# Optimization experiments

Hardware: AMD Instinct MI355X
Metric: run time of the kernel (lower is better)

## Reference

```python
import jax, jax.numpy as jnp
import numpy as np

R = 40000      # aug_num_rels
E = 500000     # number of relation-graph triplets
DIN = 64       # rel_emb_dim
DH = 64        # hid_dim_rel
H = 8          # num_head
DHID = DH // H # 8
NBIN = 10
L = 2          # num_layer_rel


def _leaky(x):
    return jax.nn.leaky_relu(x, negative_slope=0.2)


def _rel_layer(emb_rel, head, tail, binidx, pw, pb, abin, avec, aw, ab):
    # emb_rel: [R, DH]; head/tail/binidx: [E]
    concat = jnp.concatenate([emb_rel[head], emb_rel[tail]], axis=-1)  # [E, 2*DH]
    z = _leaky(concat @ pw + pb).reshape(-1, H, DHID)                   # [E, H, DHID]
    # attention logits: per-head dot with attn_vec + leaky(bin bias)
    raw = (z * avec[None]).sum(-1) + _leaky(abin[binidx, :, 0])         # [E, H]
    # segmented softmax over edges grouped by head index
    m = jax.ops.segment_max(raw, head, num_segments=R)                  # [R, H]
    e = jnp.exp(raw - m[head])                                          # [E, H]
    s = jax.ops.segment_sum(e, head, num_segments=R)                    # [R, H]
    beta = e / (s[head] + 1e-16)                                        # [E, H]
    msg = (emb_rel[tail] @ aw + ab).reshape(-1, H, DHID) * beta[..., None]
    out = jax.ops.segment_sum(msg, head, num_segments=R)                # [R, H, DHID]
    return out.reshape(R, DH)


def setup_inputs() -> dict:
    key = jax.random.key(0)
    ks = jax.random.split(key, 12)
    ht = jax.random.randint(ks[0], (E, 2), 0, R)
    b = jax.random.randint(ks[1], (E, 1), 0, NBIN)
    relation_triplets = jnp.concatenate([ht, b], axis=-1).astype(jnp.int64)
    sc = 0.05
    return {
        "relation_triplets": relation_triplets,
        "rel_emb_w": jax.random.normal(ks[2], (R, DIN), jnp.float32) * sc,
        "proj1_w": jax.random.normal(ks[3], (DIN, DH), jnp.float32) * sc,
        "proj1_b": jnp.zeros((DH,), jnp.float32),
        "attn_proj_w": jax.random.normal(ks[4], (L, 2 * DH, DH), jnp.float32) * sc,
        "attn_proj_b": jnp.zeros((L, DH), jnp.float32),
        "attn_bin": jax.random.normal(ks[5], (L, NBIN, H, 1), jnp.float32) * sc,
        "attn_vec": jax.random.normal(ks[6], (L, H, DHID), jnp.float32) * sc,
        "aggr_w": jax.random.normal(ks[7], (L, DH, DH), jnp.float32) * sc,
        "aggr_b": jnp.zeros((L, DH), jnp.float32),
        "res_w": jax.random.normal(ks[8], (L, DH, DH), jnp.float32) * sc,
        "res_b": jnp.zeros((L, DH), jnp.float32),
    }


def reference(relation_triplets, rel_emb_w, proj1_w, proj1_b, attn_proj_w,
              attn_proj_b, attn_bin, attn_vec, aggr_w, aggr_b, res_w, res_b):
    head = relation_triplets[:, 0]
    tail = relation_triplets[:, 1]
    binidx = relation_triplets[:, 2]
    emb_rel = jax.nn.relu(rel_emb_w @ proj1_w + proj1_b)  # [R, DH]
    for l in range(L):
        h = _rel_layer(emb_rel, head, tail, binidx,
                       attn_proj_w[l], attn_proj_b[l], attn_bin[l],
                       attn_vec[l], aggr_w[l], aggr_b[l])
        h = jax.nn.relu(h)
        emb_rel = h + jax.nn.relu(emb_rel @ res_w[l] + res_b[l])
    return emb_rel
```

## Files before the change

kernel.cpp:

```cpp
#include <hip/hip_runtime.h>
#include <hip/hip_bf16.h>

typedef __hip_bfloat16 bf16;

#define R_NUM 40000
#define E_NUM 500000
#define HIST_BLOCKS 1954
#define XF_BLOCKS 1250

#define PK_P1 0
#define PK_P1B 4096
#define PK_XF 4160
#define PK_AB 36928
#define PK_APB 37056
#define PK_RB 37184
#define PK_ABIN 37312
#define PK_AVEC 37472
#define PK_END 37600
#define PACK_BLOCKS 147

#define N_CNTS 0
#define N_ROWP 160000
#define N_RANK 320256
#define N_STB 2320384
#define N_FLAG 4320640
#define N_WBUF 4320896
#define N_XMP0 4471296
#define N_HR0 14711296
#define N_XMP1 35191296
#define N_HR1 45431296
#define NEED2 65911296ull

#define W_P1W 0
#define W_P1B 4096
#define W_APW 4160
#define W_APB 20544
#define W_ABIN 20672
#define W_AVEC 20832
#define W_AW 20960
#define W_AB 29152
#define W_RW 29280
#define W_RB 37472
#define W_END 37600
#define WCONV_BLOCKS 147

#define O_FLAG 0
#define O_WBUF 256
#define O_ROWP 150784
#define O_CNTS 310784
#define O_STB 635136
#define O_BIG 2635392

static __device__ __forceinline__ float b2f(bf16 x) { return __bfloat162float(x); }
static __device__ __forceinline__ float ldv(const float* p, size_t i) { return p[i]; }
static __device__ __forceinline__ float ldv(const bf16* p, size_t i) { return __bfloat162float(p[i]); }
static __device__ __forceinline__ void stv(float* p, size_t i, float v) { p[i] = v; }
static __device__ __forceinline__ void stv(bf16* p, size_t i, float v) { p[i] = __float2bfloat16(v); }

static __device__ __forceinline__ unsigned int f2bb(float x) {
  union { float f; unsigned int u; } v;
  v.f = x;
  unsigned int r = v.u + 0x7FFFu + ((v.u >> 16) & 1u);
  return r >> 16;
}
static __device__ __forceinline__ unsigned int packxm(float xt, float mt) {
  return f2bb(xt) | (f2bb(mt) << 16);
}

static __device__ __forceinline__ void load_edge(const unsigned int* __restrict__ w, int e,
                                                 int i64, int& h, int& t, int& b) {
  if (i64) {
    h = (int)w[6 * e + 0];
    t = (int)w[6 * e + 2];
    b = (int)w[6 * e + 4];
  } else {
    h = (int)w[3 * e + 0];
    t = (int)w[3 * e + 1];
    b = (int)w[3 * e + 2];
  }
}


__global__ void k_detect_init(const unsigned int* __restrict__ trip_w,
                              const unsigned short* __restrict__ emb_w, int* __restrict__ flag,
                              int* __restrict__ counts, int* __restrict__ stb) {
  int tid = threadIdx.x;
  if (blockIdx.x == 0) {
    if (tid < 64) {
      int lane = tid;
      unsigned int acc = 0;
      for (int i = lane; i < 1024; i += 64) acc |= trip_w[2 * i + 1];
      int votes = 0;
      for (int i = lane; i < 2048; i += 64) {
        unsigned short u = emb_w[2 * i];
        int ex = (u >> 7) & 0xFF;
        if (ex >= 90 && ex <= 130) votes++;
      }
      for (int off = 1; off < 64; off <<= 1) {
        acc |= __shfl_xor(acc, off);
        votes += __shfl_xor(votes, off);
      }
      if (lane == 0) {
        flag[0] = (acc == 0) ? 1 : 0;
        flag[1] = (votes < 1024) ? 1 : 0;
      }
    }
    return;
  }
  int g = (blockIdx.x - 1) * 256 + tid;
  for (int i = g; i < R_NUM; i += 159 * 256) counts[i] = 0;
  if (blockIdx.x == 1 && tid < 64) stb[E_NUM + tid] = 0;
}


__global__ void k_pack(const int* __restrict__ flag, const void* p1w, const void* p1b,
                       const void* apw, const void* apb, const void* abin, const void* avec,
                       const void* aw, const void* ab, const void* rw, const void* rb,
                       float* __restrict__ wbuf) {
  int i = blockIdx.x * 256 + threadIdx.x;
  if (i >= PK_END) return;
  const void* src;
  int off;
  if (i < PK_P1B) {
    int g = i >> 8, r = i & 255, j = r >> 2, di = r & 3;
    src = p1w;
    off = (g * 4 + di) * 64 + j;
  } else if (i < PK_XF) {
    src = p1b;
    off = i - PK_P1B;
  } else if (i < PK_AB) {
    int t = i - PK_XF;
    int l = t >> 14;
    t &= 16383;
    int g = t >> 10;
    t &= 1023;
    int m = t >> 8;
    int r = t & 255, j = r >> 2, di = r & 3;
    int ii = g * 4 + di;
    if (m == 0) { src = apw; off = l * 8192 + 4096 + ii * 64 + j; }
    else if (m == 1) { src = aw; off = l * 4096 + ii * 64 + j; }
    else if (m == 2) { src = apw; off = l * 8192 + ii * 64 + j; }
    else { src = rw; off = l * 4096 + ii * 64 + j; }
  } else if (i < PK_APB) { src = ab; off = i - PK_AB; }
  else if (i < PK_RB) { src = apb; off = i - PK_APB; }
  else if (i < PK_ABIN) { src = rb; off = i - PK_RB; }
  else if (i < PK_AVEC) { src = abin; off = i - PK_ABIN; }
  else { src = avec; off = i - PK_AVEC; }
  wbuf[i] = flag[1] ? ((const float*)src)[off] : b2f(((const bf16*)src)[off]);
}


static __device__ __forceinline__ void xf4p(const float (*sW)[64], int j, int l,
                                            const float* __restrict__ wbuf, int r0,
                                            unsigned int* __restrict__ XMp,
                                            float2* __restrict__ HR) {
  const float* W = wbuf + PK_XF + l * 16384;
  float axt[8] = {};
  float amt[8] = {};
  float axh[8] = {};
  float ars[8] = {};
  for (int g = 0; g < 16; g++) {
    const float* Wg = W + g * 1024 + j * 4;
    float4 w0 = *(const float4*)&Wg[0];
    float4 w1 = *(const float4*)&Wg[256];
    float4 w2 = *(const float4*)&Wg[512];
    float4 w3 = *(const float4*)&Wg[768];
    float4 ev[8];
#pragma unroll
    for (int n = 0; n < 8; n++) ev[n] = *(const float4*)&sW[n][g * 4];
#pragma unroll
    for (int di = 0; di < 4; di++) {
      float wt = ((const float*)&w0)[di];
      float wm = ((const float*)&w1)[di];
      float wh = ((const float*)&w2)[di];
      float wr = ((const float*)&w3)[di];
#pragma unroll
      for (int n = 0; n < 8; n++) {
        float e = ((const float*)&ev[n])[di];
        axt[n] = fmaf(e, wt, axt[n]);
        amt[n] = fmaf(e, wm, amt[n]);
        axh[n] = fmaf(e, wh, axh[n]);
        ars[n] = fmaf(e, wr, ars[n]);
      }
    }
  }
  float abj = wbuf[PK_AB + l * 64 + j];
  float pbj = wbuf[PK_APB + l * 64 + j];
  float rbj = wbuf[PK_RB + l * 64 + j];
#pragma unroll
  for (int n = 0; n < 8; n++) {
    XMp[(size_t)(r0 + n) * 64 + j] = packxm(axt[n], amt[n] + abj);
    HR[(size_t)(r0 + n) * 64 + j] = make_float2(axh[n] + pbj, fmaxf(ars[n] + rbj, 0.f));
  }
}


template <typename T>
static __device__ __forceinline__ void kA_xform(const T* __restrict__ A,
                                                const float* __restrict__ wbuf, int r0,
                                                unsigned int* __restrict__ XMp0,
                                                float2* __restrict__ HR0, float (*sW)[64]) {
  int j = threadIdx.x & 63;
  for (int k = j; k < 512; k += 64) {
    int rr = k >> 6, cc = k & 63;
    sW[rr][cc] = ldv(A, (size_t)(r0 + rr) * 64 + cc);
  }
  float a[8] = {0.f, 0.f, 0.f, 0.f, 0.f, 0.f, 0.f, 0.f};
  const float* P1 = wbuf + PK_P1;
  for (int g = 0; g < 16; g++) {
    float4 wv4 = *(const float4*)&P1[g * 256 + j * 4];
    float4 ev[8];
#pragma unroll
    for (int n = 0; n < 8; n++) ev[n] = *(const float4*)&sW[n][g * 4];
#pragma unroll
    for (int di = 0; di < 4; di++) {
      float wv = ((const float*)&wv4)[di];
#pragma unroll
      for (int n = 0; n < 8; n++) a[n] = fmaf(((const float*)&ev[n])[di], wv, a[n]);
    }
  }
  float bj = wbuf[PK_P1B + j];
#pragma unroll
  for (int n = 0; n < 8; n++) {
    a[n] = fmaxf(a[n] + bj, 0.f);
    sW[n][j] = a[n];
  }
  xf4p((const float(*)[64])sW, j, 0, wbuf, r0, XMp0, HR0);
}

__global__ void __launch_bounds__(256, 4) kA(const unsigned int* __restrict__ trip_w,
                                             const int* __restrict__ flag,
                                             const void* __restrict__ A,
                                             const float* __restrict__ wbuf,
                                             int* __restrict__ counts, int* __restrict__ rank,
                                             unsigned int* __restrict__ XMp0,
                                             float2* __restrict__ HR0) {
  if (blockIdx.x >= XF_BLOCKS) {
    int e = (blockIdx.x - XF_BLOCKS) * 256 + threadIdx.x;
    if (e < E_NUM) {
      int h = flag[0] ? (int)trip_w[6 * e] : (int)trip_w[3 * e];
      rank[e] = atomicAdd(&counts[h], 1);
    }
    return;
  }
  __shared__ float sA[32][64];
  int w = threadIdx.x >> 6;
  int r0 = blockIdx.x * 32 + w * 8;
  float(*sW)[64] = (float(*)[64]) & sA[w * 8][0];
  if (flag[1])
    kA_xform<float>((const float*)A, wbuf, r0, XMp0, HR0, sW);
  else
    kA_xform<bf16>((const bf16*)A, wbuf, r0, XMp0, HR0, sW);
}


__global__ void __launch_bounds__(1024) k_scan1(const int* __restrict__ counts,
                                                int* __restrict__ row_ptr) {
  __shared__ int sp[1024];
  int tid = threadIdx.x;
  int base = tid * 40;
  int local[40];
  int s = 0;
  if (base < R_NUM) {
#pragma unroll
    for (int k = 0; k < 40; k++) {
      int v = counts[base + k];
      local[k] = s;
      s += v;
    }
  }
  sp[tid] = s;
  __syncthreads();
  for (int off = 1; off < 1024; off <<= 1) {
    int t = (tid >= off) ? sp[tid - off] : 0;
    __syncthreads();
    sp[tid] += t;
    __syncthreads();
  }
  int pre = (tid == 0) ? 0 : sp[tid - 1];
  if (base < R_NUM) {
#pragma unroll
    for (int k = 0; k < 40; k++) row_ptr[base + k] = pre + local[k];
  }
  if (tid == 1023) row_ptr[R_NUM] = sp[1023];
}

__global__ void k_scatter2(const unsigned int* __restrict__ trip_w, const int* __restrict__ flag,
                           const int* __restrict__ row_ptr, const int* __restrict__ rank,
                           int* __restrict__ stb) {
  int e = blockIdx.x * 256 + threadIdx.x;
  if (e >= E_NUM) return;
  int h, t, b;
  load_edge(trip_w, e, flag[0], h, t, b);
  int pos = row_ptr[h] + rank[e];
  stb[pos] = (t & 0xFFFF) | (b << 16);
}


static __device__ __forceinline__ void edge_body(int l, const int* __restrict__ row_ptr,
                                                 const int* __restrict__ stb,
                                                 const unsigned int* __restrict__ XMp,
                                                 const float2* __restrict__ HR,
                                                 const float* __restrict__ wbuf,
                                                 float* __restrict__ out, float* sab) {
  int tid = threadIdx.x;
  int lane = tid & 63;
  int w = tid >> 6;
  int hh = lane >> 3;
  if (tid < 80) {
    float a = wbuf[PK_ABIN + l * 80 + tid];
    sab[tid] = (a > 0.f) ? a : 0.2f * a;
  }
  __syncthreads();
  float av = wbuf[PK_AVEC + l * 64 + lane];

  int r = blockIdx.x * 4 + w;
  float2 hr = HR[(size_t)r * 64 + lane];
  int beg = row_ptr[r];
  int end = row_ptr[r + 1];
  beg = __builtin_amdgcn_readfirstlane(beg);
  end = __builtin_amdgcn_readfirstlane(end);

  float xh = hr.x;
  float num = 0.f, den = 0.f;
  int t0 = (beg < end) ? (stb[beg] & 0xFFFF) : 0;
  for (int jj = beg; jj < end; jj += 16) {
    int pk[16];
    unsigned int xp[16];
#pragma unroll
    for (int k = 0; k < 16; k++) pk[k] = stb[jj + k];
#pragma unroll
    for (int k = 0; k < 16; k++) {
      int t = (jj + k < end) ? (pk[k] & 0xFFFF) : t0;
      xp[k] = XMp[(size_t)t * 64 + lane];
    }
#pragma unroll
    for (int k = 0; k < 16; k++) {
      float xt = __uint_as_float(xp[k] << 16);
      float mt = __uint_as_float(xp[k] & 0xFFFF0000u);
      float z = xh + xt;
      z = (z > 0.f) ? z : 0.2f * z;
      float v = z * av;
      v += __shfl_xor(v, 1);
      v += __shfl_xor(v, 2);
      v += __shfl_xor(v, 4);
      float e = __expf(v + sab[(pk[k] >> 16) * 8 + hh]);
      e = (jj + k < end) ? e : 0.f;
      den += e;
      num = fmaf(mt, e, num);
    }
  }
  out[(size_t)r * 64 + lane] = fmaxf(num / (den + 1e-16f), 0.f) + hr.y;
}

__global__ void __launch_bounds__(256, 8) kE0(const int* __restrict__ row_ptr,
                                              const int* __restrict__ stb,
                                              const unsigned int* __restrict__ XMp0,
                                              const float2* __restrict__ HR0,
                                              const float* __restrict__ wbuf,
                                              float* __restrict__ emb) {
  __shared__ float sab[80];
  edge_body(0, row_ptr, stb, XMp0, HR0, wbuf, emb, sab);
}

__global__ void __launch_bounds__(256, 8) kC(const int* __restrict__ row_ptr,
                                             const int* __restrict__ stb,
                                             const unsigned int* __restrict__ XMp1,
                                             const float2* __restrict__ HR1,
                                             const float* __restrict__ wbuf,
                                             float* __restrict__ out) {
  __shared__ float sab[80];
  edge_body(1, row_ptr, stb, XMp1, HR1, wbuf, out, sab);
}


__global__ void __launch_bounds__(256, 4) kX1(const float* __restrict__ emb,
                                              const float* __restrict__ wbuf,
                                              unsigned int* __restrict__ XMp1,
                                              float2* __restrict__ HR1) {
  __shared__ float sE[32][64];
  int j = threadIdx.x & 63;
  int w = threadIdx.x >> 6;
  int r0 = blockIdx.x * 32 + w * 8;
  float(*sW)[64] = (float(*)[64]) & sE[w * 8][0];
  for (int k = j; k < 512; k += 64) {
    int rr = k >> 6, cc = k & 63;
    sW[rr][cc] = emb[(size_t)(r0 + rr) * 64 + cc];
  }
  xf4p((const float(*)[64])sW, j, 1, wbuf, r0, XMp1, HR1);
}


__global__ void k_hist_wconv(const unsigned int* __restrict__ trip_w, const int* __restrict__ flag,
                             int* __restrict__ counts, const void* p1w, const void* p1b,
                             const void* apw, const void* apb, const void* abin, const void* avec,
                             const void* aw, const void* ab, const void* rw, const void* rb,
                             float* __restrict__ wbuf) {
  if (blockIdx.x < WCONV_BLOCKS) {
    int i = blockIdx.x * 256 + threadIdx.x;
    if (i >= W_END) return;
    const void* src;
    int off;
    if (i < W_P1B) { src = p1w; off = i - W_P1W; }
    else if (i < W_APW) { src = p1b; off = i - W_P1B; }
    else if (i < W_APB) { src = apw; off = i - W_APW; }
    else if (i < W_ABIN) { src = apb; off = i - W_APB; }
    else if (i < W_AVEC) { src = abin; off = i - W_ABIN; }
    else if (i < W_AW) { src = avec; off = i - W_AVEC; }
    else if (i < W_AB) { src = aw; off = i - W_AW; }
    else if (i < W_RW) { src = ab; off = i - W_AB; }
    else if (i < W_RB) { src = rw; off = i - W_RW; }
    else { src = rb; off = i - W_RB; }
    wbuf[i] = flag[1] ? ((const float*)src)[off] : b2f(((const bf16*)src)[off]);
    return;
  }
  int e = (blockIdx.x - WCONV_BLOCKS) * 256 + threadIdx.x;
  if (e >= E_NUM) return;
  int h, t, b;
  load_edge(trip_w, e, flag[0], h, t, b);
  atomicAdd(&counts[h], 1);
}

__global__ void k_scatter(const unsigned int* __restrict__ trip_w, const int* __restrict__ flag,
                          int* __restrict__ row_ptr, int* __restrict__ stb) {
  int e = blockIdx.x * 256 + threadIdx.x;
  if (e >= E_NUM) return;
  int h, t, b;
  load_edge(trip_w, e, flag[0], h, t, b);
  int pos = atomicAdd(&row_ptr[h], 1);
  stb[pos] = (t & 0xFFFF) | (b << 16);
}

__global__ void k_emb0(const void* __restrict__ A, const int* __restrict__ flag,
                       const float* __restrict__ wbuf, float* __restrict__ emb) {
  int j = threadIdx.x & 63;
  int g = threadIdx.x >> 6;
  int r0 = blockIdx.x * 16 + g * 4;
  int f32 = flag[1];
  __shared__ float sA[16][64];
  for (int k = threadIdx.x; k < 1024; k += 256) {
    int rr = k >> 6, cc = k & 63;
    size_t idx = (size_t)(blockIdx.x * 16 + rr) * 64 + cc;
    sA[rr][cc] = f32 ? ((const float*)A)[idx] : b2f(((const bf16*)A)[idx]);
  }
  __syncthreads();
  const float* W = wbuf + W_P1W;
  float a[4] = {0.f, 0.f, 0.f, 0.f};
  int base = g * 4;
  for (int i = 0; i < 64; i++) {
    float w = W[i * 64 + j];
#pragma unroll
    for (int n = 0; n < 4; n++) a[n] = fmaf(sA[base + n][i], w, a[n]);
  }
  float bj = wbuf[W_P1B + j];
#pragma unroll
  for (int n = 0; n < 4; n++)
    emb[(size_t)(r0 + n) * 64 + j] = fmaxf(a[n] + bj, 0.f);
}

static __device__ __forceinline__ float dotcol(const float* __restrict__ Wm, float val, int lane) {
  float acc = 0.f;
  for (int i = 0; i < 64; i++) acc = fmaf(__shfl(val, i), Wm[i * 64 + lane], acc);
  return acc;
}

template <typename TIN, typename TOUT>
__global__ void k_edge_d(const int* __restrict__ row_ptr, const int* __restrict__ stb,
                         const float* __restrict__ wbuf, int l, const TIN* __restrict__ emb_in,
                         TOUT* __restrict__ emb_out) {
  __shared__ float sab[80];
  int tid = threadIdx.x;
  int lane = tid & 63;
  int w = tid >> 6;
  int r = blockIdx.x * 4 + w;
  int hh = lane >> 3;
  if (tid < 80) {
    float a = wbuf[W_ABIN + l * 80 + tid];
    sab[tid] = (a > 0.f) ? a : 0.2f * a;
  }
  __syncthreads();
  const float* pwt = wbuf + W_APW + l * 8192;
  const float* pwb = pwt + 4096;
  const float* aw = wbuf + W_AW + l * 4096;
  const float* rw = wbuf + W_RW + l * 4096;

  float ev = ldv(emb_in, (size_t)r * 64 + lane);
  float xh = wbuf[W_APB + l * 64 + lane];
  float res = wbuf[W_RB + l * 64 + lane];
  for (int i = 0; i < 64; i++) {
    float e = __shfl(ev, i);
    xh = fmaf(e, pwt[i * 64 + lane], xh);
    res = fmaf(e, rw[i * 64 + lane], res);
  }
  res = fmaxf(res, 0.f);
  float av = wbuf[W_AVEC + l * 64 + lane];
  float abl = wbuf[W_AB + l * 64 + lane];

  int beg = (r == 0) ? 0 : row_ptr[r - 1];
  int end = row_ptr[r];
  float num = 0.f, den = 0.f;
  for (int j = beg; j < end; j++) {
    int p = stb[j];
    int t = p & 0xFFFF;
    float tv = ldv(emb_in, (size_t)t * 64 + lane);
    float z = xh + dotcol(pwb, tv, lane);
    z = (z > 0.f) ? z : 0.2f * z;
    float v = z * av;
    v += __shfl_xor(v, 1);
    v += __shfl_xor(v, 2);
    v += __shfl_xor(v, 4);
    float e = __expf(v + sab[(p >> 16) * 8 + hh]);
    den += e;
    float mt = dotcol(aw, tv, lane) + abl;
    num = fmaf(mt, e, num);
  }
  stv(emb_out, (size_t)r * 64 + lane, fmaxf(num / (den + 1e-16f), 0.f) + res);
}


extern "C" void kernel_launch(void* const* d_in, const int* in_sizes, int n_in,
                              void* d_out, int out_size, void* d_ws, size_t ws_size,
                              hipStream_t stream) {
  const unsigned int* trip_w = (const unsigned int*)d_in[0];
  const void* rel_emb = d_in[1];
  float* emb = (float*)d_out;
  char* ws = (char*)d_ws;

  if (ws_size >= NEED2) {
    int* counts = (int*)(ws + N_CNTS);
    int* row_ptr = (int*)(ws + N_ROWP);
    int* rank = (int*)(ws + N_RANK);
    int* stb = (int*)(ws + N_STB);
    int* flag = (int*)(ws + N_FLAG);
    float* wbuf = (float*)(ws + N_WBUF);
    unsigned int* XMp0 = (unsigned int*)(ws + N_XMP0);
    float2* HR0 = (float2*)(ws + N_HR0);
    unsigned int* XMp1 = (unsigned int*)(ws + N_XMP1);
    float2* HR1 = (float2*)(ws + N_HR1);

    k_detect_init<<<160, 256, 0, stream>>>(trip_w, (const unsigned short*)rel_emb, flag, counts,
                                           stb);
    k_pack<<<PACK_BLOCKS, 256, 0, stream>>>(flag, d_in[2], d_in[3], d_in[4], d_in[5], d_in[6],
                                            d_in[7], d_in[8], d_in[9], d_in[10], d_in[11], wbuf);
    kA<<<XF_BLOCKS + HIST_BLOCKS, 256, 0, stream>>>(trip_w, flag, rel_emb, wbuf, counts, rank,
                                                    XMp0, HR0);
    k_scan1<<<1, 1024, 0, stream>>>(counts, row_ptr);
    k_scatter2<<<HIST_BLOCKS, 256, 0, stream>>>(trip_w, flag, row_ptr, rank, stb);
    kE0<<<R_NUM / 4, 256, 0, stream>>>(row_ptr, stb, XMp0, HR0, wbuf, emb);
    kX1<<<XF_BLOCKS, 256, 0, stream>>>(emb, wbuf, XMp1, HR1);
    kC<<<R_NUM / 4, 256, 0, stream>>>(row_ptr, stb, XMp1, HR1, wbuf, emb);
    return;
  }

  {
    int* flag = (int*)(ws + O_FLAG);
    float* wbuf = (float*)(ws + O_WBUF);
    int* row_ptr = (int*)(ws + O_ROWP);
    int* counts = (int*)(ws + O_CNTS);
    int* stb = (int*)(ws + O_STB);
    char* big = ws + O_BIG;

    k_detect_init<<<160, 256, 0, stream>>>(trip_w, (const unsigned short*)rel_emb, flag, counts,
                                           stb);
    k_hist_wconv<<<WCONV_BLOCKS + HIST_BLOCKS, 256, 0, stream>>>(
        trip_w, flag, counts, d_in[2], d_in[3], d_in[4], d_in[5], d_in[6], d_in[7], d_in[8],
        d_in[9], d_in[10], d_in[11], wbuf);
    k_scan1<<<1, 1024, 0, stream>>>(counts, row_ptr);
    k_scatter<<<HIST_BLOCKS, 256, 0, stream>>>(trip_w, flag, row_ptr, stb);
    k_emb0<<<R_NUM / 16, 256, 0, stream>>>(rel_emb, flag, wbuf, emb);
    bf16* embB = (bf16*)big;
    k_edge_d<float, bf16><<<R_NUM / 4, 256, 0, stream>>>(row_ptr, stb, wbuf, 0, emb, embB);
    k_edge_d<bf16, float><<<R_NUM / 4, 256, 0, stream>>>(row_ptr, stb, wbuf, 1, embB, emb);
  }
}
```

Baseline: 232.8 us.

## Merge detect and pack kernels, stage transform weights in shared memory

Combines the format-detect/zero-init kernel and the weight-pack kernel into one launch: each pack block recomputes the dtype vote locally, which removes one kernel launch and its dependency. The per-row transform kernels (kA, kX1) now cooperatively copy weight chunks into a 16KB shared buffer with block barriers, instead of each thread reading float4 weights from global memory. This cuts redundant global/L2 weight traffic, but adds 16KB LDS per block and extra __syncthreads, which may lower occupancy.

```diff
diff --git a/kernel.cpp b/kernel.cpp
--- a/kernel.cpp
+++ b/kernel.cpp
@@ -7,6 +7,7 @@
 #define E_NUM 500000
 #define HIST_BLOCKS 1954
 #define XF_BLOCKS 1250
+#define ZERO_BLOCKS 157
 
 #define PK_P1 0
 #define PK_P1B 4096
@@ -18,6 +19,7 @@
 #define PK_AVEC 37472
 #define PK_END 37600
 #define PACK_BLOCKS 147
+#define INIT_BLOCKS (PACK_BLOCKS + ZERO_BLOCKS)
 
 #define N_CNTS 0
 #define N_ROWP 160000
@@ -78,6 +80,336 @@
     t = (int)w[3 * e + 1];
     b = (int)w[3 * e + 2];
   }
+}
+
+
+__global__ void __launch_bounds__(256) k_init(
+    const unsigned int* __restrict__ trip_w, const unsigned short* __restrict__ emb16,
+    int* __restrict__ flag, int* __restrict__ counts, int* __restrict__ stb, const void* p1w,
+    const void* p1b, const void* apw, const void* apb, const void* abin, const void* avec,
+    const void* aw, const void* ab, const void* rw, const void* rb, float* __restrict__ wbuf) {
+  int tid = threadIdx.x;
+  int bid = blockIdx.x;
+  if (bid < PACK_BLOCKS) {
+    __shared__ int sfl;
+    if (tid < 64) {
+      unsigned int acc = 0;
+      for (int i = tid; i < 1024; i += 64) acc |= trip_w[2 * i + 1];
+      int votes = 0;
+      for (int i = tid; i < 2048; i += 64) {
+        unsigned short u = emb16[2 * i];
+        int ex = (u >> 7) & 0xFF;
+        if (ex >= 90 && ex <= 130) votes++;
+      }
+      for (int off = 1; off < 64; off <<= 1) {
+        acc |= __shfl_xor(acc, off);
+        votes += __shfl_xor(votes, off);
+      }
+      if (tid == 0) {
+        sfl = (votes < 1024) ? 1 : 0;
+        if (bid == 0) {
+          flag[0] = (acc == 0) ? 1 : 0;
+          flag[1] = sfl;
+        }
+      }
+    }
+    __syncthreads();
+    int f32w = sfl;
+    int i = bid * 256 + tid;
+    if (i >= PK_END) return;
+    const void* src;
+    int off;
+    if (i < PK_P1B) {
+      int g = i >> 8, r = i & 255, j = r >> 2, di = r & 3;
+      src = p1w;
+      off = (g * 4 + di) * 64 + j;
+    } else if (i < PK_XF) {
+      src = p1b;
+      off = i - PK_P1B;
+    } else if (i < PK_AB) {
+      int t = i - PK_XF;
+      int l = t >> 14;
+      t &= 16383;
+      int g = t >> 10;
+      t &= 1023;
+      int m = t >> 8;
+      int r = t & 255, j = r >> 2, di = r & 3;
+      int ii = g * 4 + di;
+      if (m == 0) { src = apw; off = l * 8192 + 4096 + ii * 64 + j; }
+      else if (m == 1) { src = aw; off = l * 4096 + ii * 64 + j; }
+      else if (m == 2) { src = apw; off = l * 8192 + ii * 64 + j; }
+      else { src = rw; off = l * 4096 + ii * 64 + j; }
+    } else if (i < PK_APB) { src = ab; off = i - PK_AB; }
+    else if (i < PK_RB) { src = apb; off = i - PK_APB; }
+    else if (i < PK_ABIN) { src = rb; off = i - PK_RB; }
+    else if (i < PK_AVEC) { src = abin; off = i - PK_ABIN; }
+    else { src = avec; off = i - PK_AVEC; }
+    wbuf[i] = f32w ? ((const float*)src)[off] : b2f(((const bf16*)src)[off]);
+    return;
+  }
+  int g = (bid - PACK_BLOCKS) * 256 + tid;
+  if (g < R_NUM) counts[g] = 0;
+  if (bid == PACK_BLOCKS && tid < 64) stb[E_NUM + tid] = 0;
+}
+
+
+static __device__ __forceinline__ void xf4s(const float (*sW)[64], float* __restrict__ sWt,
+                                            int tid, int l, const float* __restrict__ wbuf,
+                                            int r0, unsigned int* __restrict__ XMp,
+                                            float2* __restrict__ HR) {
+  int j = tid & 63;
+  float axt[8] = {};
+  float amt[8] = {};
+  float axh[8] = {};
+  float ars[8] = {};
+  for (int c = 0; c < 4; c++) {
+    __syncthreads();
+    {
+      const float4* src = (const float4*)(wbuf + PK_XF + l * 16384 + c * 4096);
+      float4* dst = (float4*)sWt;
+      for (int k = tid; k < 1024; k += 256) dst[k] = src[k];
+    }
+    __syncthreads();
+#pragma unroll
+    for (int gg = 0; gg < 4; gg++) {
+      int g = c * 4 + gg;
+      const float* Wg = sWt + gg * 1024 + j * 4;
+      float4 w0 = *(const float4*)&Wg[0];
+      float4 w1 = *(const float4*)&Wg[256];
+      float4 w2 = *(const float4*)&Wg[512];
+      float4 w3 = *(const float4*)&Wg[768];
+      float4 ev[8];
+#pragma unroll
+      for (int n = 0; n < 8; n++) ev[n] = *(const float4*)&sW[n][g * 4];
+#pragma unroll
+      for (int di = 0; di < 4; di++) {
+        float wt = ((const float*)&w0)[di];
+        float wm = ((const float*)&w1)[di];
+        float wh = ((const float*)&w2)[di];
+        float wr = ((const float*)&w3)[di];
+#pragma unroll
+        for (int n = 0; n < 8; n++) {
+          float e = ((const float*)&ev[n])[di];
+          axt[n] = fmaf(e, wt, axt[n]);
+          amt[n] = fmaf(e, wm, amt[n]);
+          axh[n] = fmaf(e, wh, axh[n]);
+          ars[n] = fmaf(e, wr, ars[n]);
+        }
+      }
+    }
+  }
+  float abj = wbuf[PK_AB + l * 64 + j];
+  float pbj = wbuf[PK_APB + l * 64 + j];
+  float rbj = wbuf[PK_RB + l * 64 + j];
+#pragma unroll
+  for (int n = 0; n < 8; n++) {
+    XMp[(size_t)(r0 + n) * 64 + j] = packxm(axt[n], amt[n] + abj);
+    HR[(size_t)(r0 + n) * 64 + j] = make_float2(axh[n] + pbj, fmaxf(ars[n] + rbj, 0.f));
+  }
+}
+
+
+template <typename T>
+static __device__ __forceinline__ void kA_xform(const T* __restrict__ A,
+                                                const float* __restrict__ wbuf, int r0,
+                                                unsigned int* __restrict__ XMp0,
+                                                float2* __restrict__ HR0, float (*sW)[64],
+                                                float* __restrict__ sWt, int tid) {
+  int j = tid & 63;
+  for (int k = j; k < 512; k += 64) {
+    sW[k >> 6][k & 63] = ldv(A, (size_t)(r0 + (k >> 6)) * 64 + (k & 63));
+  }
+  {
+    const float4* src = (const float4*)(wbuf + PK_P1);
+    float4* dst = (float4*)sWt;
+    for (int k = tid; k < 1024; k += 256) dst[k] = src[k];
+  }
+  __syncthreads();
+  float a[8] = {0.f, 0.f, 0.f, 0.f, 0.f, 0.f, 0.f, 0.f};
+  for (int g = 0; g < 16; g++) {
+    float4 wv4 = *(const float4*)&sWt[g * 256 + j * 4];
+    float4 ev[8];
+#pragma unroll
+    for (int n = 0; n < 8; n++) ev[n] = *(const float4*)&sW[n][g * 4];
+#pragma unroll
+    for (int di = 0; di < 4; di++) {
+      float wv = ((const float*)&wv4)[di];
+#pragma unroll
+      for (int n = 0; n < 8; n++) a[n] = fmaf(((const float*)&ev[n])[di], wv, a[n]);
+    }
+  }
+  float bj = wbuf[PK_P1B + j];
+#pragma unroll
+  for (int n = 0; n < 8; n++) {
+    a[n] = fmaxf(a[n] + bj, 0.f);
+    sW[n][j] = a[n];
+  }
+  xf4s((const float(*)[64])sW, sWt, tid, 0, wbuf, r0, XMp0, HR0);
+}
+
+__global__ void __launch_bounds__(256, 4) kA(const unsigned int* __restrict__ trip_w,
+                                             const int* __restrict__ flag,
+                                             const void* __restrict__ A,
+                                             const float* __restrict__ wbuf,
+                                             int* __restrict__ counts, int* __restrict__ rank,
+                                             unsigned int* __restrict__ XMp0,
+                                             float2* __restrict__ HR0) {
+  if (blockIdx.x >= XF_BLOCKS) {
+    int e = (blockIdx.x - XF_BLOCKS) * 256 + threadIdx.x;
+    if (e < E_NUM) {
+      int h = flag[0] ? (int)trip_w[6 * e] : (int)trip_w[3 * e];
+      rank[e] = atomicAdd(&counts[h], 1);
+    }
+    return;
+  }
+  __shared__ float sA[32][64];
+  __shared__ float sWt[4096];
+  int tid = threadIdx.x;
+  int w = tid >> 6;
+  int r0 = blockIdx.x * 32 + w * 8;
+  float(*sW)[64] = (float(*)[64]) & sA[w * 8][0];
+  if (flag[1])
+    kA_xform<float>((const float*)A, wbuf, r0, XMp0, HR0, sW, sWt, tid);
+  else
+    kA_xform<bf16>((const bf16*)A, wbuf, r0, XMp0, HR0, sW, sWt, tid);
+}
+
+
+__global__ void __launch_bounds__(1024) k_scan1(const int* __restrict__ counts,
+                                                int* __restrict__ row_ptr) {
+  __shared__ int sp[1024];
+  int tid = threadIdx.x;
+  int base = tid * 40;
+  int local[40];
+  int s = 0;
+  if (base < R_NUM) {
+#pragma unroll
+    for (int k = 0; k < 40; k++) {
+      int v = counts[base + k];
+      local[k] = s;
+      s += v;
+    }
+  }
+  sp[tid] = s;
+  __syncthreads();
+  for (int off = 1; off < 1024; off <<= 1) {
+    int t = (tid >= off) ? sp[tid - off] : 0;
+    __syncthreads();
+    sp[tid] += t;
+    __syncthreads();
+  }
+  int pre = (tid == 0) ? 0 : sp[tid - 1];
+  if (base < R_NUM) {
+#pragma unroll
+    for (int k = 0; k < 40; k++) row_ptr[base + k] = pre + local[k];
+  }
+  if (tid == 1023) row_ptr[R_NUM] = sp[1023];
+}
+
+__global__ void k_scatter2(const unsigned int* __restrict__ trip_w, const int* __restrict__ flag,
+                           const int* __restrict__ row_ptr, const int* __restrict__ rank,
+                           int* __restrict__ stb) {
+  int e = blockIdx.x * 256 + threadIdx.x;
+  if (e >= E_NUM) return;
+  int h, t, b;
+  load_edge(trip_w, e, flag[0], h, t, b);
+  int pos = row_ptr[h] + rank[e];
+  stb[pos] = (t & 0xFFFF) | (b << 16);
+}
+
+
+static __device__ __forceinline__ void edge_body(int l, const int* __restrict__ row_ptr,
+                                                 const int* __restrict__ stb,
+                                                 const unsigned int* __restrict__ XMp,
+                                                 const float2* __restrict__ HR,
+                                                 const float* __restrict__ wbuf,
+                                                 float* __restrict__ out, float* sab) {
+  int tid = threadIdx.x;
+  int lane = tid & 63;
+  int w = tid >> 6;
+  int hh = lane >> 3;
+  if (tid < 80) {
+    float a = wbuf[PK_ABIN + l * 80 + tid];
+    sab[tid] = (a > 0.f) ? a : 0.2f * a;
+  }
+  __syncthreads();
+  float av = wbuf[PK_AVEC + l * 64 + lane];
+
+  int r = blockIdx.x * 4 + w;
+  float2 hr = HR[(size_t)r * 64 + lane];
+  int beg = row_ptr[r];
+  int end = row_ptr[r + 1];
+  beg = __builtin_amdgcn_readfirstlane(beg);
+  end = __builtin_amdgcn_readfirstlane(end);
+
+  float xh = hr.x;
+  float num = 0.f, den = 0.f;
+  int t0 = (beg < end) ? (stb[beg] & 0xFFFF) : 0;
+  for (int jj = beg; jj < end; jj += 16) {
+    int pk[16];
+    unsigned int xp[16];
+#pragma unroll
+    for (int k = 0; k < 16; k++) pk[k] = stb[jj + k];
+#pragma unroll
+    for (int k = 0; k < 16; k++) {
+      int t = (jj + k < end) ? (pk[k] & 0xFFFF) : t0;
+      xp[k] = XMp[(size_t)t * 64 + lane];
+    }
+#pragma unroll
+    for (int k = 0; k < 16; k++) {
+      float xt = __uint_as_float(xp[k] << 16);
+      float mt = __uint_as_float(xp[k] & 0xFFFF0000u);
+      float z = xh + xt;
+      z = (z > 0.f) ? z : 0.2f * z;
+      float v = z * av;
+      v += __shfl_xor(v, 1);
+      v += __shfl_xor(v, 2);
+      v += __shfl_xor(v, 4);
+      float e = __expf(v + sab[(pk[k] >> 16) * 8 + hh]);
+      e = (jj + k < end) ? e : 0.f;
+      den += e;
+      num = fmaf(mt, e, num);
+    }
+  }
+  out[(size_t)r * 64 + lane] = fmaxf(num / (den + 1e-16f), 0.f) + hr.y;
+}
+
+__global__ void __launch_bounds__(256, 8) kE0(const int* __restrict__ row_ptr,
+                                              const int* __restrict__ stb,
+                                              const unsigned int* __restrict__ XMp0,
+                                              const float2* __restrict__ HR0,
+                                              const float* __restrict__ wbuf,
+                                              float* __restrict__ emb) {
+  __shared__ float sab[80];
+  edge_body(0, row_ptr, stb, XMp0, HR0, wbuf, emb, sab);
+}
+
+__global__ void __launch_bounds__(256, 8) kC(const int* __restrict__ row_ptr,
+                                             const int* __restrict__ stb,
+                                             const unsigned int* __restrict__ XMp1,
+                                             const float2* __restrict__ HR1,
+                                             const float* __restrict__ wbuf,
+                                             float* __restrict__ out) {
+  __shared__ float sab[80];
+  edge_body(1, row_ptr, stb, XMp1, HR1, wbuf, out, sab);
+}
+
+
+__global__ void __launch_bounds__(256, 4) kX1(const float* __restrict__ emb,
+                                              const float* __restrict__ wbuf,
+                                              unsigned int* __restrict__ XMp1,
+                                              float2* __restrict__ HR1) {
+  __shared__ float sE[32][64];
+  __shared__ float sWt[4096];
+  int tid = threadIdx.x;
+  int j = tid & 63;
+  int w = tid >> 6;
+  int r0 = blockIdx.x * 32 + w * 8;
+  float(*sW)[64] = (float(*)[64]) & sE[w * 8][0];
+  for (int k = j; k < 512; k += 64) {
+    sW[k >> 6][k & 63] = emb[(size_t)(r0 + (k >> 6)) * 64 + (k & 63)];
+  }
+  xf4s((const float(*)[64])sW, sWt, tid, 1, wbuf, r0, XMp1, HR1);
 }
 
 
@@ -112,285 +444,6 @@
   if (blockIdx.x == 1 && tid < 64) stb[E_NUM + tid] = 0;
 }
 
-
-__global__ void k_pack(const int* __restrict__ flag, const void* p1w, const void* p1b,
-                       const void* apw, const void* apb, const void* abin, const void* avec,
-                       const void* aw, const void* ab, const void* rw, const void* rb,
-                       float* __restrict__ wbuf) {
-  int i = blockIdx.x * 256 + threadIdx.x;
-  if (i >= PK_END) return;
-  const void* src;
-  int off;
-  if (i < PK_P1B) {
-    int g = i >> 8, r = i & 255, j = r >> 2, di = r & 3;
-    src = p1w;
-    off = (g * 4 + di) * 64 + j;
-  } else if (i < PK_XF) {
-    src = p1b;
-    off = i - PK_P1B;
-  } else if (i < PK_AB) {
-    int t = i - PK_XF;
-    int l = t >> 14;
-    t &= 16383;
-    int g = t >> 10;
-    t &= 1023;
-    int m = t >> 8;
-    int r = t & 255, j = r >> 2, di = r & 3;
-    int ii = g * 4 + di;
-    if (m == 0) { src = apw; off = l * 8192 + 4096 + ii * 64 + j; }
-    else if (m == 1) { src = aw; off = l * 4096 + ii * 64 + j; }
-    else if (m == 2) { src = apw; off = l * 8192 + ii * 64 + j; }
-    else { src = rw; off = l * 4096 + ii * 64 + j; }
-  } else if (i < PK_APB) { src = ab; off = i - PK_AB; }
-  else if (i < PK_RB) { src = apb; off = i - PK_APB; }
-  else if (i < PK_ABIN) { src = rb; off = i - PK_RB; }
-  else if (i < PK_AVEC) { src = abin; off = i - PK_ABIN; }
-  else { src = avec; off = i - PK_AVEC; }
-  wbuf[i] = flag[1] ? ((const float*)src)[off] : b2f(((const bf16*)src)[off]);
-}
-
-
-static __device__ __forceinline__ void xf4p(const float (*sW)[64], int j, int l,
-                                            const float* __restrict__ wbuf, int r0,
-                                            unsigned int* __restrict__ XMp,
-                                            float2* __restrict__ HR) {
-  const float* W = wbuf + PK_XF + l * 16384;
-  float axt[8] = {};
-  float amt[8] = {};
-  float axh[8] = {};
-  float ars[8] = {};
-  for (int g = 0; g < 16; g++) {
-    const float* Wg = W + g * 1024 + j * 4;
-    float4 w0 = *(const float4*)&Wg[0];
-    float4 w1 = *(const float4*)&Wg[256];
-    float4 w2 = *(const float4*)&Wg[512];
-    float4 w3 = *(const float4*)&Wg[768];
-    float4 ev[8];
-#pragma unroll
-    for (int n = 0; n < 8; n++) ev[n] = *(const float4*)&sW[n][g * 4];
-#pragma unroll
-    for (int di = 0; di < 4; di++) {
-      float wt = ((const float*)&w0)[di];
-      float wm = ((const float*)&w1)[di];
-      float wh = ((const float*)&w2)[di];
-      float wr = ((const float*)&w3)[di];
-#pragma unroll
-      for (int n = 0; n < 8; n++) {
-        float e = ((const float*)&ev[n])[di];
-        axt[n] = fmaf(e, wt, axt[n]);
-        amt[n] = fmaf(e, wm, amt[n]);
-        axh[n] = fmaf(e, wh, axh[n]);
-        ars[n] = fmaf(e, wr, ars[n]);
-      }
-    }
-  }
-  float abj = wbuf[PK_AB + l * 64 + j];
-  float pbj = wbuf[PK_APB + l * 64 + j];
-  float rbj = wbuf[PK_RB + l * 64 + j];
-#pragma unroll
-  for (int n = 0; n < 8; n++) {
-    XMp[(size_t)(r0 + n) * 64 + j] = packxm(axt[n], amt[n] + abj);
-    HR[(size_t)(r0 + n) * 64 + j] = make_float2(axh[n] + pbj, fmaxf(ars[n] + rbj, 0.f));
-  }
-}
-
-
-template <typename T>
-static __device__ __forceinline__ void kA_xform(const T* __restrict__ A,
-                                                const float* __restrict__ wbuf, int r0,
-                                                unsigned int* __restrict__ XMp0,
-                                                float2* __restrict__ HR0, float (*sW)[64]) {
-  int j = threadIdx.x & 63;
-  for (int k = j; k < 512; k += 64) {
-    int rr = k >> 6, cc = k & 63;
-    sW[rr][cc] = ldv(A, (size_t)(r0 + rr) * 64 + cc);
-  }
-  float a[8] = {0.f, 0.f, 0.f, 0.f, 0.f, 0.f, 0.f, 0.f};
-  const float* P1 = wbuf + PK_P1;
-  for (int g = 0; g < 16; g++) {
-    float4 wv4 = *(const float4*)&P1[g * 256 + j * 4];
-    float4 ev[8];
-#pragma unroll
-    for (int n = 0; n < 8; n++) ev[n] = *(const float4*)&sW[n][g * 4];
-#pragma unroll
-    for (int di = 0; di < 4; di++) {
-      float wv = ((const float*)&wv4)[di];
-#pragma unroll
-      for (int n = 0; n < 8; n++) a[n] = fmaf(((const float*)&ev[n])[di], wv, a[n]);
-    }
-  }
-  float bj = wbuf[PK_P1B + j];
-#pragma unroll
-  for (int n = 0; n < 8; n++) {
-    a[n] = fmaxf(a[n] + bj, 0.f);
-    sW[n][j] = a[n];
-  }
-  xf4p((const float(*)[64])sW, j, 0, wbuf, r0, XMp0, HR0);
-}
-
-__global__ void __launch_bounds__(256, 4) kA(const unsigned int* __restrict__ trip_w,
-                                             const int* __restrict__ flag,
-                                             const void* __restrict__ A,
-                                             const float* __restrict__ wbuf,
-                                             int* __restrict__ counts, int* __restrict__ rank,
-                                             unsigned int* __restrict__ XMp0,
-                                             float2* __restrict__ HR0) {
-  if (blockIdx.x >= XF_BLOCKS) {
-    int e = (blockIdx.x - XF_BLOCKS) * 256 + threadIdx.x;
-    if (e < E_NUM) {
-      int h = flag[0] ? (int)trip_w[6 * e] : (int)trip_w[3 * e];
-      rank[e] = atomicAdd(&counts[h], 1);
-    }
-    return;
-  }
-  __shared__ float sA[32][64];
-  int w = threadIdx.x >> 6;
-  int r0 = blockIdx.x * 32 + w * 8;
-  float(*sW)[64] = (float(*)[64]) & sA[w * 8][0];
-  if (flag[1])
-    kA_xform<float>((const float*)A, wbuf, r0, XMp0, HR0, sW);
-  else
-    kA_xform<bf16>((const bf16*)A, wbuf, r0, XMp0, HR0, sW);
-}
-
-
-__global__ void __launch_bounds__(1024) k_scan1(const int* __restrict__ counts,
-                                                int* __restrict__ row_ptr) {
-  __shared__ int sp[1024];
-  int tid = threadIdx.x;
-  int base = tid * 40;
-  int local[40];
-  int s = 0;
-  if (base < R_NUM) {
-#pragma unroll
-    for (int k = 0; k < 40; k++) {
-      int v = counts[base + k];
-      local[k] = s;
-      s += v;
-    }
-  }
-  sp[tid] = s;
-  __syncthreads();
-  for (int off = 1; off < 1024; off <<= 1) {
-    int t = (tid >= off) ? sp[tid - off] : 0;
-    __syncthreads();
-    sp[tid] += t;
-    __syncthreads();
-  }
-  int pre = (tid == 0) ? 0 : sp[tid - 1];
-  if (base < R_NUM) {
-#pragma unroll
-    for (int k = 0; k < 40; k++) row_ptr[base + k] = pre + local[k];
-  }
-  if (tid == 1023) row_ptr[R_NUM] = sp[1023];
-}
-
-__global__ void k_scatter2(const unsigned int* __restrict__ trip_w, const int* __restrict__ flag,
-                           const int* __restrict__ row_ptr, const int* __restrict__ rank,
-                           int* __restrict__ stb) {
-  int e = blockIdx.x * 256 + threadIdx.x;
-  if (e >= E_NUM) return;
-  int h, t, b;
-  load_edge(trip_w, e, flag[0], h, t, b);
-  int pos = row_ptr[h] + rank[e];
-  stb[pos] = (t & 0xFFFF) | (b << 16);
-}
-
-
-static __device__ __forceinline__ void edge_body(int l, const int* __restrict__ row_ptr,
-                                                 const int* __restrict__ stb,
-                                                 const unsigned int* __restrict__ XMp,
-                                                 const float2* __restrict__ HR,
-                                                 const float* __restrict__ wbuf,
-                                                 float* __restrict__ out, float* sab) {
-  int tid = threadIdx.x;
-  int lane = tid & 63;
-  int w = tid >> 6;
-  int hh = lane >> 3;
-  if (tid < 80) {
-    float a = wbuf[PK_ABIN + l * 80 + tid];
-    sab[tid] = (a > 0.f) ? a : 0.2f * a;
-  }
-  __syncthreads();
-  float av = wbuf[PK_AVEC + l * 64 + lane];
-
-  int r = blockIdx.x * 4 + w;
-  float2 hr = HR[(size_t)r * 64 + lane];
-  int beg = row_ptr[r];
-  int end = row_ptr[r + 1];
-  beg = __builtin_amdgcn_readfirstlane(beg);
-  end = __builtin_amdgcn_readfirstlane(end);
-
-  float xh = hr.x;
-  float num = 0.f, den = 0.f;
-  int t0 = (beg < end) ? (stb[beg] & 0xFFFF) : 0;
-  for (int jj = beg; jj < end; jj += 16) {
-    int pk[16];
-    unsigned int xp[16];
-#pragma unroll
-    for (int k = 0; k < 16; k++) pk[k] = stb[jj + k];
-#pragma unroll
-    for (int k = 0; k < 16; k++) {
-      int t = (jj + k < end) ? (pk[k] & 0xFFFF) : t0;
-      xp[k] = XMp[(size_t)t * 64 + lane];
-    }
-#pragma unroll
-    for (int k = 0; k < 16; k++) {
-      float xt = __uint_as_float(xp[k] << 16);
-      float mt = __uint_as_float(xp[k] & 0xFFFF0000u);
-      float z = xh + xt;
-      z = (z > 0.f) ? z : 0.2f * z;
-      float v = z * av;
-      v += __shfl_xor(v, 1);
-      v += __shfl_xor(v, 2);
-      v += __shfl_xor(v, 4);
-      float e = __expf(v + sab[(pk[k] >> 16) * 8 + hh]);
-      e = (jj + k < end) ? e : 0.f;
-      den += e;
-      num = fmaf(mt, e, num);
-    }
-  }
-  out[(size_t)r * 64 + lane] = fmaxf(num / (den + 1e-16f), 0.f) + hr.y;
-}
-
-__global__ void __launch_bounds__(256, 8) kE0(const int* __restrict__ row_ptr,
-                                              const int* __restrict__ stb,
-                                              const unsigned int* __restrict__ XMp0,
-                                              const float2* __restrict__ HR0,
-                                              const float* __restrict__ wbuf,
-                                              float* __restrict__ emb) {
-  __shared__ float sab[80];
-  edge_body(0, row_ptr, stb, XMp0, HR0, wbuf, emb, sab);
-}
-
-__global__ void __launch_bounds__(256, 8) kC(const int* __restrict__ row_ptr,
-                                             const int* __restrict__ stb,
-                                             const unsigned int* __restrict__ XMp1,
-                                             const float2* __restrict__ HR1,
-                                             const float* __restrict__ wbuf,
-                                             float* __restrict__ out) {
-  __shared__ float sab[80];
-  edge_body(1, row_ptr, stb, XMp1, HR1, wbuf, out, sab);
-}
-
-
-__global__ void __launch_bounds__(256, 4) kX1(const float* __restrict__ emb,
-                                              const float* __restrict__ wbuf,
-                                              unsigned int* __restrict__ XMp1,
-                                              float2* __restrict__ HR1) {
-  __shared__ float sE[32][64];
-  int j = threadIdx.x & 63;
-  int w = threadIdx.x >> 6;
-  int r0 = blockIdx.x * 32 + w * 8;
-  float(*sW)[64] = (float(*)[64]) & sE[w * 8][0];
-  for (int k = j; k < 512; k += 64) {
-    int rr = k >> 6, cc = k & 63;
-    sW[rr][cc] = emb[(size_t)(r0 + rr) * 64 + cc];
-  }
-  xf4p((const float(*)[64])sW, j, 1, wbuf, r0, XMp1, HR1);
-}
-
-
 __global__ void k_hist_wconv(const unsigned int* __restrict__ trip_w, const int* __restrict__ flag,
                              int* __restrict__ counts, const void* p1w, const void* p1b,
                              const void* apw, const void* apb, const void* abin, const void* avec,
@@ -538,9 +591,8 @@
     unsigned int* XMp1 = (unsigned int*)(ws + N_XMP1);
     float2* HR1 = (float2*)(ws + N_HR1);
 
-    k_detect_init<<<160, 256, 0, stream>>>(trip_w, (const unsigned short*)rel_emb, flag, counts,
-                                           stb);
-    k_pack<<<PACK_BLOCKS, 256, 0, stream>>>(flag, d_in[2], d_in[3], d_in[4], d_in[5], d_in[6],
+    k_init<<<INIT_BLOCKS, 256, 0, stream>>>(trip_w, (const unsigned short*)rel_emb, flag, counts,
+                                            stb, d_in[2], d_in[3], d_in[4], d_in[5], d_in[6],
                                             d_in[7], d_in[8], d_in[9], d_in[10], d_in[11], wbuf);
     kA<<<XF_BLOCKS + HIST_BLOCKS, 256, 0, stream>>>(trip_w, flag, rel_emb, wbuf, counts, rank,
                                                     XMp0, HR0);
```

Result: slower. 270.0 us (+16.0%).
